# Kernel tuning notes

Measured on AMD Instinct MI355X. Metric: run time of the kernel, lower is better.

Reference implementation:

```python
import jax, jax.numpy as jnp
import numpy as np

N = 200_000      # nodes
E = 6_400_000    # edges (avg degree 32)
ATT = 16         # scorer hidden dim
MAXD = 512       # mixer max_depth
C = 1.0          # curvature
EPS = 1e-15


def _mobius_add(a, b, c):
    # Mobius addition on the Poincare ball: a (+)_c b
    ab = jnp.sum(a * b, axis=-1, keepdims=True)
    aa = jnp.sum(a * a, axis=-1, keepdims=True)
    bb = jnp.sum(b * b, axis=-1, keepdims=True)
    num = (1.0 + 2.0 * c * ab + c * bb) * a + (1.0 - c * aa) * b
    den = 1.0 + 2.0 * c * ab + (c * c) * aa * bb
    return num / jnp.maximum(den, EPS)


def setup_inputs() -> dict:
    key = jax.random.key(0)
    ks = jax.random.split(key, 8)
    x = jax.random.normal(ks[0], (N, 2), dtype=jnp.float32)
    # keep nodes strictly inside the unit Poincare disk (|x| < 0.5)
    x = 0.5 * x / (1.0 + jnp.linalg.norm(x, axis=-1, keepdims=True))
    edge_index = jax.random.randint(ks[1], (2, E), 0, N, dtype=jnp.int32)
    depth = jax.random.randint(ks[2], (N,), 0, MAXD, dtype=jnp.int32)
    W1 = jax.random.normal(ks[3], (2, ATT), dtype=jnp.float32) * (1.0 / np.sqrt(2.0))
    b1 = jnp.zeros((ATT,), dtype=jnp.float32)
    W2 = jax.random.normal(ks[4], (ATT, 1), dtype=jnp.float32) * (1.0 / np.sqrt(ATT))
    eta = jnp.array(1.0, dtype=jnp.float32)
    depth_scale = 1.0 + 0.1 * jax.random.normal(ks[5], (MAXD, 1), dtype=jnp.float32)
    depth_theta = 0.1 * jax.random.normal(ks[6], (MAXD, 1), dtype=jnp.float32)
    return dict(x=x, edge_index=edge_index, depth=depth, W1=W1, b1=b1, W2=W2,
                eta=eta, depth_scale=depth_scale, depth_theta=depth_theta)


def reference(x, edge_index, depth, W1, b1, W2, eta, depth_scale, depth_theta):
    c = C
    sc = jnp.sqrt(jnp.asarray(c, dtype=x.dtype))
    row, col = edge_index[0], edge_index[1]
    xi = x[row]   # [E,2] target node of each edge
    xj = x[col]   # [E,2] source node of each edge

    # log_{xi}(xj): tangent vector at xi
    u = _mobius_add(-xi, xj, c)                                        # [E,2]
    un = jnp.maximum(jnp.linalg.norm(u, axis=-1, keepdims=True), EPS)  # [E,1]
    lam_i = 2.0 / jnp.maximum(1.0 - c * jnp.sum(xi * xi, axis=-1, keepdims=True), EPS)
    v = (2.0 / (sc * lam_i)) * jnp.arctanh(jnp.minimum(sc * un, 1.0 - 1e-5)) * (u / un)

    # tiny MLP attention score per edge
    h = jax.nn.gelu(v @ W1 + b1, approximate=False)   # [E,ATT]
    scores = (h @ W2)[:, 0]                           # [E]

    # segment softmax over edges grouped by target node `row`
    smax = jax.ops.segment_max(scores, row, num_segments=N)
    ex = jnp.exp(scores - smax[row])
    denom = jax.ops.segment_sum(ex, row, num_segments=N)
    alpha = ex / jnp.maximum(denom[row], 1e-15)       # [E]

    # weighted scatter-add of tangent vectors
    m = jax.ops.segment_sum(alpha[:, None] * v, row, num_segments=N)   # [N,2]

    # depth-gated rotation/scale in the tangent space (mixer)
    d = jnp.clip(depth, 0, MAXD - 1)
    k = depth_scale[d]            # [N,1]
    ang = depth_theta[d][:, 0]    # [N]
    ca, sa = jnp.cos(ang), jnp.sin(ang)
    m = k * jnp.stack([ca * m[:, 0] - sa * m[:, 1],
                       sa * m[:, 0] + ca * m[:, 1]], axis=-1)

    # exp_{x}(eta * m)
    w = eta * m
    wn = jnp.maximum(jnp.linalg.norm(w, axis=-1, keepdims=True), EPS)
    lam_x = 2.0 / jnp.maximum(1.0 - c * jnp.sum(x * x, axis=-1, keepdims=True), EPS)
    second = jnp.tanh(sc * lam_x * wn / 2.0) * (w / (sc * wn))
    return _mobius_add(x, second, c)
```

## Files before the change

kernel.cpp:

```cpp
#include <hip/hip_runtime.h>
#include <hip/hip_fp16.h>
#include <math.h>

#define EPSF 1e-15f
#define BSH  8
#define BSZ  (1 << BSH)
#define BMSK (BSZ - 1)
#define CAPB 9216
#define MAXNB 1024
#define AGG_T 1024
#define BIN_T 1024
#define LCH   6400

#define TBL   128
#define TW    129
#define VMIN  (-1.2f)
#define VH    (2.4f / 128.0f)
#define INVH  (128.0f / 2.4f)

__device__ __forceinline__ float fast_rcp(float x)  { return __builtin_amdgcn_rcpf(x); }
__device__ __forceinline__ float fast_rsq(float x)  { return __builtin_amdgcn_rsqf(x); }
__device__ __forceinline__ float fast_exp(float x)  { return __builtin_amdgcn_exp2f(x * 1.4426950408889634f); }

__device__ __forceinline__ unsigned int float_to_ordered(float f) {
    unsigned int u = __float_as_uint(f);
    return (u & 0x80000000u) ? ~u : (u | 0x80000000u);
}
__device__ __forceinline__ float ordered_to_float(unsigned int u) {
    u = (u & 0x80000000u) ? (u & 0x7FFFFFFFu) : ~u;
    return __uint_as_float(u);
}

__device__ __forceinline__ void edge_v_fast(float2 xi, float2 xj, float& vx, float& vy) {
    float ab = -(xi.x * xj.x + xi.y * xj.y);
    float aa = xi.x * xi.x + xi.y * xi.y;
    float bb = xj.x * xj.x + xj.y * xj.y;
    float f1 = 1.0f + 2.0f * ab + bb;
    float f2 = 1.0f - aa;
    float ux = f1 * (-xi.x) + f2 * xj.x;
    float uy = f1 * (-xi.y) + f2 * xj.y;
    float den = 1.0f + 2.0f * ab + aa * bb;
    float inv_den = fast_rcp(fmaxf(den, EPSF));
    ux *= inv_den; uy *= inv_den;
    float un2 = fmaxf(ux * ux + uy * uy, 1e-24f);
    float inv_un = fast_rsq(un2);
    float un = fminf(un2 * inv_un, 1.0f - 1e-5f);
    float t = 0.34657359027997264f * __builtin_amdgcn_logf((1.0f + un) * fast_rcp(1.0f - un));
    float s = fmaxf(f2, EPSF) * t * inv_un;
    vx = s * ux; vy = s * uy;
}

__device__ __forceinline__ void edge_v(float2 xi, float2 xj, float& vx, float& vy) {
    float ab = -(xi.x * xj.x + xi.y * xj.y);
    float aa = xi.x * xi.x + xi.y * xi.y;
    float bb = xj.x * xj.x + xj.y * xj.y;
    float f1 = 1.0f + 2.0f * ab + bb;
    float f2 = 1.0f - aa;
    float ux = f1 * (-xi.x) + f2 * xj.x;
    float uy = f1 * (-xi.y) + f2 * xj.y;
    float den = 1.0f + 2.0f * ab + aa * bb;
    float inv_den = 1.0f / fmaxf(den, EPSF);
    ux *= inv_den; uy *= inv_den;
    float un = fmaxf(sqrtf(ux * ux + uy * uy), EPSF);
    float t  = atanhf(fminf(un, 1.0f - 1e-5f));
    float s = fmaxf(f2, EPSF) * t / un;
    vx = s * ux; vy = s * uy;
}

__device__ __forceinline__ float edge_score(float vx, float vy,
                                            const float* __restrict__ W1,
                                            const float* __restrict__ b1,
                                            const float* __restrict__ W2) {
    float score = 0.0f;
#pragma unroll
    for (int k = 0; k < 16; ++k) {
        float z = fmaf(vx, W1[k], fmaf(vy, W1[16 + k], b1[k]));
        float g = 0.5f * z * (1.0f + erff(z * 0.70710678118654752f));
        score = fmaf(g, W2[k], score);
    }
    return score;
}

__device__ __forceinline__ float2 finalize_node(float2 xv, float mx, float my,
                                                int d, float eta,
                                                const float* __restrict__ dscale,
                                                const float* __restrict__ dtheta) {
    d = d < 0 ? 0 : (d > 511 ? 511 : d);
    float k   = dscale[d];
    float ang = dtheta[d];
    float ca = cosf(ang), sa = sinf(ang);
    float m0 = k * (ca * mx - sa * my);
    float m1 = k * (sa * mx + ca * my);

    float wx = eta * m0, wy = eta * m1;
    float wn = fmaxf(sqrtf(wx * wx + wy * wy), 1e-15f);

    float aa = xv.x * xv.x + xv.y * xv.y;
    float lam = 2.0f / fmaxf(1.0f - aa, 1e-15f);
    float fac = tanhf(lam * wn * 0.5f) / wn;
    float sx = fac * wx, sy = fac * wy;

    float ab = xv.x * sx + xv.y * sy;
    float bb = sx * sx + sy * sy;
    float n1 = 1.0f + 2.0f * ab + bb;
    float n2 = 1.0f - aa;
    float ox = n1 * xv.x + n2 * sx;
    float oy = n1 * xv.y + n2 * sy;
    float dd = 1.0f + 2.0f * ab + aa * bb;
    float inv = 1.0f / fmaxf(dd, 1e-15f);
    return make_float2(ox * inv, oy * inv);
}


__global__ void init_cursor(unsigned* __restrict__ cursor, int NB) {
    int b = blockIdx.x * blockDim.x + threadIdx.x;
    if (b < NB) cursor[b] = (unsigned)b * CAPB;
}

__global__ void build_score_table(const float* __restrict__ W1,
                                  const float* __restrict__ b1,
                                  const float* __restrict__ W2,
                                  float* __restrict__ tbl) {
    int i = blockIdx.x * blockDim.x + threadIdx.x;
    if (i >= TW * TW) return;
    int iy = i / TW, ix = i - iy * TW;
    float vx = VMIN + VH * (float)ix;
    float vy = VMIN + VH * (float)iy;
    tbl[i] = edge_score(vx, vy, W1, b1, W2);
}

__global__ __launch_bounds__(BIN_T)
void bin_edges(const int* __restrict__ ei,
               unsigned* __restrict__ cursor,
               unsigned* __restrict__ sorted,
               int E, int NB) {
    __shared__ unsigned bkrank[LCH];
    __shared__ unsigned payload[LCH];
    __shared__ unsigned sortedLoc[LCH];
    __shared__ unsigned gdst[LCH];
    __shared__ unsigned hist[MAXNB];
    __shared__ unsigned scanA[MAXNB];
    __shared__ unsigned loc[MAXNB];
    __shared__ unsigned gbase[MAXNB];

    int tid = threadIdx.x;
    int e0 = blockIdx.x * LCH;
    int cnt = min(E - e0, LCH);
    if (cnt <= 0) return;

    if (tid < MAXNB) hist[tid] = 0;
    __syncthreads();

    for (int idx = tid; idx < cnt; idx += BIN_T) {
        int r = ei[e0 + idx];
        int c = ei[E + e0 + idx];
        unsigned bk = (unsigned)r >> BSH;
        unsigned rank = atomicAdd(&hist[bk], 1u);
        bkrank[idx] = (bk << 14) | rank;
        payload[idx] = ((unsigned)(r & BMSK) << 24) | (unsigned)c;
    }
    __syncthreads();

    unsigned h = (tid < MAXNB) ? hist[tid] : 0u;
    if (tid < MAXNB) scanA[tid] = h;
    __syncthreads();
#pragma unroll
    for (int step = 1; step < MAXNB; step <<= 1) {
        unsigned v = 0u;
        if (tid < MAXNB) {
            v = scanA[tid];
            if (tid >= step) v += scanA[tid - step];
        }
        __syncthreads();
        if (tid < MAXNB) scanA[tid] = v;
        __syncthreads();
    }
    if (tid < MAXNB) {
        loc[tid] = scanA[tid] - h;
        gbase[tid] = h ? atomicAdd(&cursor[tid], h) : 0u;
    }
    __syncthreads();

    for (int idx = tid; idx < cnt; idx += BIN_T) {
        unsigned v = bkrank[idx];
        unsigned bk = v >> 14;
        unsigned rank = v & 0x3FFFu;
        unsigned pos = loc[bk] + rank;
        sortedLoc[pos] = payload[idx];
        unsigned g = gbase[bk] + rank;
        gdst[pos] = (g < (bk + 1u) * CAPB) ? g : 0xFFFFFFFFu;
    }
    __syncthreads();

    for (int idx = tid; idx < cnt; idx += BIN_T) {
        unsigned g = gdst[idx];
        if (g != 0xFFFFFFFFu) sorted[g] = sortedLoc[idx];
    }
}

__global__ __launch_bounds__(AGG_T, 8)
void aggregate(const float2* __restrict__ x,
               const unsigned* __restrict__ cursor,
               const unsigned* __restrict__ sorted,
               const int* __restrict__ depth,
               const float* __restrict__ tbl,
               const float* __restrict__ etaPtr,
               const float* __restrict__ dscale,
               const float* __restrict__ dtheta,
               float2* __restrict__ out, int N) {
    __shared__ float2 xr[BSZ];
    __shared__ unsigned stashA[CAPB];
    __shared__ unsigned stashV[CAPB];
    __shared__ unsigned nmax[BSZ];
    __shared__ unsigned long long accP[BSZ];

    int b = blockIdx.x;
    int tid = threadIdx.x;
    int nb0 = b << BSH;
    int nodeCnt = min(BSZ, N - nb0);
    if (tid < BSZ) {
        nmax[tid] = 0u;
        accP[tid] = 0ull;
        if (tid < nodeCnt) xr[tid] = x[nb0 + tid];
    }
    __syncthreads();

    unsigned basep = (unsigned)b * CAPB;
    unsigned cnt = cursor[b] - basep;
    cnt = cnt > (unsigned)CAPB ? (unsigned)CAPB : cnt;

    for (unsigned i = tid; i < cnt; i += AGG_T) {
        unsigned u = sorted[basep + i];
        int rl = (int)(u >> 24);
        int c  = (int)(u & 0xFFFFFFu);
        float2 xi = xr[rl];
        float2 xj = x[c];
        float vx, vy;
        edge_v_fast(xi, xj, vx, vy);

        float tx = fminf(fmaxf((vx - VMIN) * INVH, 0.0f), 127.999f);
        float ty = fminf(fmaxf((vy - VMIN) * INVH, 0.0f), 127.999f);
        int ix = (int)tx, iy = (int)ty;
        float fx = tx - (float)ix, fy = ty - (float)iy;
        const float* row = tbl + iy * TW + ix;
        float s00 = row[0], s01 = row[1];
        float s10 = row[TW], s11 = row[TW + 1];
        float sA = fmaf(fx, s01 - s00, s00);
        float sB = fmaf(fx, s11 - s10, s10);
        float score = fmaf(fy, sB - sA, sA);

        __half hs = __float2half_rn(score);
        float sq = __half2float(hs);
        unsigned short s16 = *(unsigned short*)&hs;
        __half2 h2 = __floats2half2_rn(vx, vy);
        stashA[i] = ((unsigned)rl << 16) | (unsigned)s16;
        stashV[i] = *(unsigned*)&h2;
        atomicMax(&nmax[rl], float_to_ordered(sq));
    }
    __syncthreads();

    for (unsigned i = tid; i < cnt; i += AGG_T) {
        unsigned a = stashA[i];
        int rl = (int)(a >> 16);
        unsigned short s16 = (unsigned short)(a & 0xFFFFu);
        __half hs = *(__half*)&s16;
        float s = __half2float(hs);
        float mxs = ordered_to_float(nmax[rl]);
        float ex = fast_exp(s - mxs);
        unsigned vv = stashV[i];
        __half2 h2 = *(__half2*)&vv;
        float2 v2 = __half22float2(h2);
        unsigned e0 = __float2uint_rn(ex * 16384.0f);
        unsigned e1 = __float2uint_rn(ex * (v2.x + 2.0f) * 0.25f * 16384.0f);
        unsigned e2 = __float2uint_rn(ex * (v2.y + 2.0f) * 0.25f * 16384.0f);
        unsigned long long pk = (unsigned long long)e0
                              | ((unsigned long long)e1 << 21)
                              | ((unsigned long long)e2 << 42);
        atomicAdd(&accP[rl], pk);
    }
    __syncthreads();

    if (tid >= nodeCnt) return;
    unsigned long long w = accP[tid];
    float F0 = (float)(unsigned int)(w & 0x1FFFFFull);
    float F1 = (float)(unsigned int)((w >> 21) & 0x1FFFFFull);
    float F2 = (float)(unsigned int)(w >> 42);
    float mx = 0.0f, my = 0.0f;
    if (F0 > 0.0f) {
        float inv = 1.0f / F0;
        mx = 4.0f * F1 * inv - 2.0f;
        my = 4.0f * F2 * inv - 2.0f;
    }
    int i = nb0 + tid;
    out[i] = finalize_node(xr[tid], mx, my, depth[i], etaPtr[0], dscale, dtheta);
}


__global__ void init_kernel(unsigned int* __restrict__ smax,
                            unsigned long long* __restrict__ maccP, int N) {
    int i = blockIdx.x * blockDim.x + threadIdx.x;
    if (i < N) {
        smax[i] = float_to_ordered(-INFINITY);
        maccP[i] = 0ull;
    }
}

__global__ void pass1_score_max(const float2* __restrict__ x,
                                const int* __restrict__ ei,
                                const float* __restrict__ W1,
                                const float* __restrict__ b1,
                                const float* __restrict__ W2,
                                unsigned int* __restrict__ smax, int E) {
    int e = blockIdx.x * blockDim.x + threadIdx.x;
    if (e >= E) return;
    int r = ei[e];
    int c = ei[E + e];
    float vx, vy;
    edge_v(x[r], x[c], vx, vy);
    float score = edge_score(vx, vy, W1, b1, W2);
    atomicMax(&smax[r], float_to_ordered(score));
}

#define PK_SCALE 16384.0f

__global__ void pass2_accum(const float2* __restrict__ x,
                            const int* __restrict__ ei,
                            const float* __restrict__ W1,
                            const float* __restrict__ b1,
                            const float* __restrict__ W2,
                            const unsigned int* __restrict__ smax,
                            unsigned long long* __restrict__ maccP, int E) {
    int e = blockIdx.x * blockDim.x + threadIdx.x;
    if (e >= E) return;
    int r = ei[e];
    int c = ei[E + e];
    float vx, vy;
    edge_v(x[r], x[c], vx, vy);
    float score = edge_score(vx, vy, W1, b1, W2);
    float mx = ordered_to_float(smax[r]);
    float ex = expf(score - mx);
    unsigned e0 = __float2uint_rn(ex * PK_SCALE);
    unsigned e1 = __float2uint_rn(ex * (vx + 2.0f) * 0.25f * PK_SCALE);
    unsigned e2 = __float2uint_rn(ex * (vy + 2.0f) * 0.25f * PK_SCALE);
    unsigned long long pk = (unsigned long long)e0
                          | ((unsigned long long)e1 << 21)
                          | ((unsigned long long)e2 << 42);
    atomicAdd(&maccP[r], pk);
}

__global__ void pass3_finalize(const float2* __restrict__ x,
                               const int* __restrict__ depth,
                               const unsigned long long* __restrict__ maccP,
                               const float* __restrict__ etaPtr,
                               const float* __restrict__ dscale,
                               const float* __restrict__ dtheta,
                               float2* __restrict__ out, int N) {
    int i = blockIdx.x * blockDim.x + threadIdx.x;
    if (i >= N) return;
    unsigned long long w = maccP[i];
    float F0 = (float)(unsigned int)(w & 0x1FFFFFull);
    float F1 = (float)(unsigned int)((w >> 21) & 0x1FFFFFull);
    float F2 = (float)(unsigned int)(w >> 42);
    float mx = 0.0f, my = 0.0f;
    if (F0 > 0.0f) {
        float inv = 1.0f / F0;
        mx = 4.0f * F1 * inv - 2.0f;
        my = 4.0f * F2 * inv - 2.0f;
    }
    out[i] = finalize_node(x[i], mx, my, depth[i], etaPtr[0], dscale, dtheta);
}


extern "C" void kernel_launch(void* const* d_in, const int* in_sizes, int n_in,
                              void* d_out, int out_size, void* d_ws, size_t ws_size,
                              hipStream_t stream) {
    const float2* x   = (const float2*)d_in[0];
    const int* ei     = (const int*)d_in[1];
    const int* depth  = (const int*)d_in[2];
    const float* W1   = (const float*)d_in[3];
    const float* b1   = (const float*)d_in[4];
    const float* W2   = (const float*)d_in[5];
    const float* eta  = (const float*)d_in[6];
    const float* dsc  = (const float*)d_in[7];
    const float* dth  = (const float*)d_in[8];
    float2* out = (float2*)d_out;

    int N = in_sizes[0] / 2;
    int E = in_sizes[1] / 2;
    int NB = (N + BSZ - 1) >> BSH;

    const int B = 256;
    size_t sortedBytes = (size_t)NB * CAPB * 4;
    size_t need = 4096 + sortedBytes + (size_t)TW * TW * 4;
    if (NB <= MAXNB && ws_size >= need) {
        unsigned* cursor = (unsigned*)d_ws;
        unsigned* sorted = (unsigned*)((char*)d_ws + 4096);
        float* tbl = (float*)((char*)d_ws + 4096 + sortedBytes);
        int binG = (E + LCH - 1) / LCH;
        init_cursor<<<(NB + B - 1) / B, B, 0, stream>>>(cursor, NB);
        build_score_table<<<(TW * TW + B - 1) / B, B, 0, stream>>>(W1, b1, W2, tbl);
        bin_edges<<<binG, BIN_T, 0, stream>>>(ei, cursor, sorted, E, NB);
        aggregate<<<NB, AGG_T, 0, stream>>>(x, cursor, sorted, depth, tbl,
                                            eta, dsc, dth, out, N);
    } else {
        unsigned long long* maccP = (unsigned long long*)d_ws;
        unsigned int* smax = (unsigned int*)(maccP + N);
        init_kernel<<<(N + B - 1) / B, B, 0, stream>>>(smax, maccP, N);
        pass1_score_max<<<(E + B - 1) / B, B, 0, stream>>>(x, ei, W1, b1, W2, smax, E);
        pass2_accum<<<(E + B - 1) / B, B, 0, stream>>>(x, ei, W1, b1, W2, smax, maccP, E);
        pass3_finalize<<<(N + B - 1) / B, B, 0, stream>>>(x, depth, maccP, eta, dsc, dth, out, N);
    }
}
```

Before: 195.2 us.

## Drop local sort in binning, pack score table as half2 pairs, enlarge chunk

The binning kernel no longer runs a shared-memory prefix scan and local reorder before writing. Each edge is now scattered straight to its global bucket slot, which removes several barriers and the scan. The score lookup table now holds horizontally adjacent entries as fp16 pairs, so bilinear interpolation needs two loads instead of four, at some cost in precision. The edge chunk per binning block grows from 6400 to 8192. The global writes become less coalesced because the local sort that grouped them by bucket is gone.

```diff
diff --git a/kernel.cpp b/kernel.cpp
--- a/kernel.cpp
+++ b/kernel.cpp
@@ -10,10 +10,11 @@
 #define MAXNB 1024
 #define AGG_T 1024
 #define BIN_T 1024
-#define LCH   6400
+#define LCH   8192
 
 #define TBL   128
 #define TW    129
+#define TP    128
 #define VMIN  (-1.2f)
 #define VH    (2.4f / 128.0f)
 #define INVH  (128.0f / 2.4f)
@@ -120,13 +121,15 @@
 __global__ void build_score_table(const float* __restrict__ W1,
                                   const float* __restrict__ b1,
                                   const float* __restrict__ W2,
-                                  float* __restrict__ tbl) {
+                                  __half2* __restrict__ tblP) {
     int i = blockIdx.x * blockDim.x + threadIdx.x;
-    if (i >= TW * TW) return;
-    int iy = i / TW, ix = i - iy * TW;
-    float vx = VMIN + VH * (float)ix;
+    if (i >= TW * TP) return;
+    int iy = i / TP, ix = i - iy * TP;
     float vy = VMIN + VH * (float)iy;
-    tbl[i] = edge_score(vx, vy, W1, b1, W2);
+    float vx0 = VMIN + VH * (float)ix;
+    float s0 = edge_score(vx0, vy, W1, b1, W2);
+    float s1 = edge_score(vx0 + VH, vy, W1, b1, W2);
+    tblP[i] = __floats2half2_rn(s0, s1);
 }
 
 __global__ __launch_bounds__(BIN_T)
@@ -136,11 +139,7 @@
                int E, int NB) {
     __shared__ unsigned bkrank[LCH];
     __shared__ unsigned payload[LCH];
-    __shared__ unsigned sortedLoc[LCH];
-    __shared__ unsigned gdst[LCH];
     __shared__ unsigned hist[MAXNB];
-    __shared__ unsigned scanA[MAXNB];
-    __shared__ unsigned loc[MAXNB];
     __shared__ unsigned gbase[MAXNB];
 
     int tid = threadIdx.x;
@@ -156,45 +155,24 @@
         int c = ei[E + e0 + idx];
         unsigned bk = (unsigned)r >> BSH;
         unsigned rank = atomicAdd(&hist[bk], 1u);
-        bkrank[idx] = (bk << 14) | rank;
+        bkrank[idx] = (bk << 13) | rank;
         payload[idx] = ((unsigned)(r & BMSK) << 24) | (unsigned)c;
     }
     __syncthreads();
 
-    unsigned h = (tid < MAXNB) ? hist[tid] : 0u;
-    if (tid < MAXNB) scanA[tid] = h;
-    __syncthreads();
-#pragma unroll
-    for (int step = 1; step < MAXNB; step <<= 1) {
-        unsigned v = 0u;
-        if (tid < MAXNB) {
-            v = scanA[tid];
-            if (tid >= step) v += scanA[tid - step];
-        }
-        __syncthreads();
-        if (tid < MAXNB) scanA[tid] = v;
-        __syncthreads();
-    }
     if (tid < MAXNB) {
-        loc[tid] = scanA[tid] - h;
+        unsigned h = hist[tid];
         gbase[tid] = h ? atomicAdd(&cursor[tid], h) : 0u;
     }
     __syncthreads();
 
     for (int idx = tid; idx < cnt; idx += BIN_T) {
         unsigned v = bkrank[idx];
-        unsigned bk = v >> 14;
-        unsigned rank = v & 0x3FFFu;
-        unsigned pos = loc[bk] + rank;
-        sortedLoc[pos] = payload[idx];
+        unsigned bk = v >> 13;
+        unsigned rank = v & 0x1FFFu;
         unsigned g = gbase[bk] + rank;
-        gdst[pos] = (g < (bk + 1u) * CAPB) ? g : 0xFFFFFFFFu;
-    }
-    __syncthreads();
-
-    for (int idx = tid; idx < cnt; idx += BIN_T) {
-        unsigned g = gdst[idx];
-        if (g != 0xFFFFFFFFu) sorted[g] = sortedLoc[idx];
+        if (g < (bk + 1u) * CAPB)
+            sorted[g] = payload[idx];
     }
 }
 
@@ -203,7 +181,7 @@
                const unsigned* __restrict__ cursor,
                const unsigned* __restrict__ sorted,
                const int* __restrict__ depth,
-               const float* __restrict__ tbl,
+               const __half2* __restrict__ tblP,
                const float* __restrict__ etaPtr,
                const float* __restrict__ dscale,
                const float* __restrict__ dtheta,
@@ -242,11 +220,10 @@
         float ty = fminf(fmaxf((vy - VMIN) * INVH, 0.0f), 127.999f);
         int ix = (int)tx, iy = (int)ty;
         float fx = tx - (float)ix, fy = ty - (float)iy;
-        const float* row = tbl + iy * TW + ix;
-        float s00 = row[0], s01 = row[1];
-        float s10 = row[TW], s11 = row[TW + 1];
-        float sA = fmaf(fx, s01 - s00, s00);
-        float sB = fmaf(fx, s11 - s10, s10);
+        float2 r0 = __half22float2(tblP[iy * TP + ix]);
+        float2 r1 = __half22float2(tblP[(iy + 1) * TP + ix]);
+        float sA = fmaf(fx, r0.y - r0.x, r0.x);
+        float sB = fmaf(fx, r1.y - r1.x, r1.x);
         float score = fmaf(fy, sB - sA, sA);
 
         __half hs = __float2half_rn(score);
@@ -391,16 +368,16 @@
 
     const int B = 256;
     size_t sortedBytes = (size_t)NB * CAPB * 4;
-    size_t need = 4096 + sortedBytes + (size_t)TW * TW * 4;
+    size_t need = 4096 + sortedBytes + (size_t)TW * TP * 4;
     if (NB <= MAXNB && ws_size >= need) {
         unsigned* cursor = (unsigned*)d_ws;
         unsigned* sorted = (unsigned*)((char*)d_ws + 4096);
-        float* tbl = (float*)((char*)d_ws + 4096 + sortedBytes);
+        __half2* tblP = (__half2*)((char*)d_ws + 4096 + sortedBytes);
         int binG = (E + LCH - 1) / LCH;
         init_cursor<<<(NB + B - 1) / B, B, 0, stream>>>(cursor, NB);
-        build_score_table<<<(TW * TW + B - 1) / B, B, 0, stream>>>(W1, b1, W2, tbl);
+        build_score_table<<<(TW * TP + B - 1) / B, B, 0, stream>>>(W1, b1, W2, tblP);
         bin_edges<<<binG, BIN_T, 0, stream>>>(ei, cursor, sorted, E, NB);
-        aggregate<<<NB, AGG_T, 0, stream>>>(x, cursor, sorted, depth, tbl,
+        aggregate<<<NB, AGG_T, 0, stream>>>(x, cursor, sorted, depth, tblP,
                                             eta, dsc, dth, out, N);
     } else {
         unsigned long long* maccP = (unsigned long long*)d_ws;
```

After: 207.2 us. +6.1%, slower.
